# Kernel optimization log

Hardware: AMD Instinct MI355X
Metric: run time of the kernel (lower is better)

The kernel has to match this reference:

```python
import jax, jax.numpy as jnp
import numpy as np

DN = ('NCHW', 'OIHW', 'NCHW')

def conv2d(x, w, b):
    y = jax.lax.conv_general_dilated(x, w, window_strides=(1, 1), padding='SAME', dimension_numbers=DN)
    return y + b[None, :, None, None]

def setup_inputs() -> dict:
    key = jax.random.key(0)
    ks = jax.random.split(key, 8)
    C = 256
    Cq = C // 8
    B, H, W = 8, 56, 56
    fan_out_qk = Cq * 9
    fan_out_v = C * 9
    std_qk = np.sqrt(2.0 / fan_out_qk)  # kaiming_normal fan_out, relu
    std_v = np.sqrt(2.0 / fan_out_v)
    return {
        'x': jax.random.normal(ks[0], (B, C, H, W), dtype=jnp.float32),
        'wq': jax.random.normal(ks[1], (Cq, C, 3, 3), dtype=jnp.float32) * std_qk,
        'bq': jnp.zeros((Cq,), dtype=jnp.float32),
        'wk': jax.random.normal(ks[2], (Cq, C, 3, 3), dtype=jnp.float32) * std_qk,
        'bk': jnp.zeros((Cq,), dtype=jnp.float32),
        'wv': jax.random.normal(ks[3], (C, C, 3, 3), dtype=jnp.float32) * std_v,
        'bv': jnp.zeros((C,), dtype=jnp.float32),
        'gamma': jax.random.uniform(ks[4], (1,), dtype=jnp.float32) * 0.1,
    }

def reference(x, wq, bq, wk, bk, wv, bv, gamma):
    B, C, H, W = x.shape
    N = H * W
    q = conv2d(x, wq, bq).reshape(B, -1, N)   # [B, C/8, N]
    k = conv2d(x, wk, bk).reshape(B, -1, N)   # [B, C/8, N]
    v = conv2d(x, wv, bv).reshape(B, C, N)    # [B, C, N]
    # energy[b,i,j] = sum_d q[b,d,i] * k[b,d,j]  (unscaled)
    energy = jnp.einsum('bdi,bdj->bij', q, k)
    attention = jax.nn.softmax(energy, axis=-1)  # [B, N, N]
    # out[b,c,i] = sum_j v[b,c,j] * attention[b,i,j]
    out = jnp.einsum('bcj,bij->bci', v, attention).reshape(B, C, H, W)
    return gamma[0] * out + x
```

## Files before the change

### kernel.cpp

```cpp
#include <hip/hip_runtime.h>
#include <math.h>

#define B_ 8
#define C_ 256
#define H_ 56
#define W_ 56
#define N_ 3136
#define BN_ (B_*N_)
#define LOG2E 1.44269504088896340736f

typedef __attribute__((ext_vector_type(8))) short short8;
typedef __attribute__((ext_vector_type(4))) float f32x4;
typedef __attribute__((ext_vector_type(16))) float f32x16;
typedef __attribute__((ext_vector_type(4))) unsigned short u16x4;
#define MFMA16(A, Bf, Cf) __builtin_amdgcn_mfma_f32_16x16x32_bf16((A), (Bf), (Cf), 0, 0, 0)
#define MFMA32(A, Bf, Cf) __builtin_amdgcn_mfma_f32_32x32x16_bf16((A), (Bf), (Cf), 0, 0, 0)

#define XT_ELEMS (B_*58*64*256)
#define A_ELEMS  (320*2304)
#define AHI_OFF  (2*XT_ELEMS)
#define ALO_OFF  (AHI_OFF + A_ELEMS)
#define QKT_HI_OFF (ALO_OFF + A_ELEMS)
#define QKT_ELEMS  (B_*N_*64)
#define QKT_LO_OFF (QKT_HI_OFF + QKT_ELEMS)
#define VBF_OFF    (QKT_LO_OFF + QKT_ELEMS)
#define VBF_ELEMS  (B_*C_*N_)

#define QF_ELEMS (B_*196*64*8)


#define SX(col) ((((col) & 3)) ^ (((col) >> 2) & 3))
#define SWZ(r, col, c8) ((((r)*64 + (col))*4) + ((c8) ^ SX(col)))

#define PSTR 76
#define VSTR 58

__device__ inline unsigned short f2bf(float f) {
    unsigned u = __float_as_uint(f);
    unsigned r = (u + 0x7fffu + ((u >> 16) & 1u)) >> 16;
    return (unsigned short)r;
}
__device__ inline float bf2f(unsigned short h) {
    return __uint_as_float(((unsigned)h) << 16);
}
__device__ inline float exp2_hw(float x) {
    float r; asm("v_exp_f32 %0, %1" : "=v"(r) : "v"(x)); return r;
}
__device__ inline unsigned cvt_pk_bf16(float lo, float hi) {
    unsigned r; asm("v_cvt_pk_bf16_f32 %0, %1, %2" : "=v"(r) : "v"(lo), "v"(hi)); return r;
}
__device__ inline void gl_lds16(const unsigned short* g, uint4* l) {
    __builtin_amdgcn_global_load_lds(
        (const __attribute__((address_space(1))) unsigned int*)g,
        (__attribute__((address_space(3))) unsigned int*)l,
        16, 0, 0);
}

__global__ __launch_bounds__(256) void zero_pads(
    unsigned short* __restrict__ xhi, unsigned short* __restrict__ xlo)
{
    const int g = blockIdx.x*256 + threadIdx.x;
    const int half = 61440;
    unsigned short* base = (g < half) ? xhi : xlo;
    const int i = (g < half) ? g : g - half;
    const int b = i / 7680, rem = i - b*7680;
    const int slot = rem >> 5, c8 = rem & 31;
    int row, col;
    if (slot < 64)       { row = 0;  col = slot; }
    else if (slot < 128) { row = 57; col = slot - 64; }
    else if (slot < 184) { row = slot - 127; col = 0; }
    else                 { row = slot - 183; col = 57; }
    const size_t o = ((size_t)((b*58 + row)*64 + col))*256 + c8*8;
    *(uint4*)(base + o) = make_uint4(0, 0, 0, 0);
}

__global__ __launch_bounds__(256) void prep_x(
    const float* __restrict__ x,
    unsigned short* __restrict__ xhi, unsigned short* __restrict__ xlo)
{
    __shared__ float xs[64][57];
    const int cc = blockIdx.x, y = blockIdx.y, b = blockIdx.z;
    const int t = threadIdx.x;
    const int c0 = cc * 64;
    for (int idx = t; idx < 64 * 56; idx += 256) {
        const int ch = idx / 56, xc = idx - ch * 56;
        xs[ch][xc] = x[((size_t)(b*C_ + c0 + ch)*H_ + y)*W_ + xc];
    }
    __syncthreads();
    for (int idx = t; idx < 56 * 32; idx += 256) {
        const int xc = idx >> 5, chp = idx & 31;
        const float v0 = xs[2*chp][xc], v1 = xs[2*chp + 1][xc];
        const unsigned short h0 = f2bf(v0), h1 = f2bf(v1);
        const unsigned short l0 = f2bf(v0 - bf2f(h0));
        const unsigned short l1 = f2bf(v1 - bf2f(h1));
        const size_t o = ((size_t)(b*58 + y + 1) * 64 + (xc + 1)) * 256 + c0 + 2*chp;
        *(unsigned*)(xhi + o) = (unsigned)h0 | ((unsigned)h1 << 16);
        *(unsigned*)(xlo + o) = (unsigned)l0 | ((unsigned)l1 << 16);
    }
}

__global__ __launch_bounds__(256) void prep_w(
    const float* __restrict__ wq, const float* __restrict__ wk,
    const float* __restrict__ wv,
    unsigned short* __restrict__ Ahi, unsigned short* __restrict__ Alo)
{
    const int g = blockIdx.x * 256 + threadIdx.x;
    if (g >= 320 * 2304) return;
    const int m = g / 2304, k = g - m * 2304;
    const int s = k >> 8, c = k & 255;
    float w;
    if (m < 32)      w = wq[((size_t)m*C_ + c)*9 + s];
    else if (m < 64) w = wk[((size_t)(m-32)*C_ + c)*9 + s];
    else             w = wv[((size_t)(m-64)*C_ + c)*9 + s];
    const unsigned short h = f2bf(w);
    const int cc = (k >> 5) & 7, quad = (k >> 3) & 3, e = k & 7;
    const size_t o = ((((size_t)(m >> 4)*9 + s)*8 + cc)*64 + (quad*16 + (m & 15)))*8 + e;
    Ahi[o] = h;
    Alo[o] = f2bf(w - bf2f(h));
}

__global__ __launch_bounds__(256, 3) void conv_fused(
    const unsigned short* __restrict__ xhi, const unsigned short* __restrict__ xlo,
    const unsigned short* __restrict__ Ahi, const unsigned short* __restrict__ Alo,
    const float* __restrict__ bq, const float* __restrict__ bk,
    const float* __restrict__ bv,
    unsigned short* __restrict__ qkt_hi, unsigned short* __restrict__ qkt_lo,
    unsigned short* __restrict__ vbf)
{
    __shared__ uint4 SMEM[3080];
    const int b = blockIdx.x, y = blockIdx.y, z = blockIdx.z;
    const int t = threadIdx.x;
    const int w = t >> 6, L = t & 63;
    const int ln = L & 15, quad = L >> 4;

    size_t gofs[3];
#pragma unroll
    for (int i = 0; i < 3; i++) {
        const int ci = w*192 + i*64 + L;
        const int r = ci >> 8, col = (ci >> 2) & 63;
        const int c8 = (ci & 3) ^ SX(col);
        gofs[i] = ((size_t)((b*58 + y + r)*64 + col))*256 + c8*8;
    }

    if (z == 0) {
        const int wrg = w >> 1, wnt = w & 1;
        f32x4 acc[2][2];
#pragma unroll
        for (int i = 0; i < 2; i++) { acc[i][0] = (f32x4)0.0f; acc[i][1] = (f32x4)0.0f; }

#pragma unroll
        for (int i = 0; i < 3; i++) {
            gl_lds16(xhi + gofs[i], SMEM + w*192 + i*64);
            gl_lds16(xlo + gofs[i], SMEM + 768 + w*192 + i*64);
        }
        __syncthreads();

        for (int cc = 0; cc < 8; cc++) {
            const int buf = cc & 1;
            const uint4* sH = SMEM + buf*1536;
            const uint4* sL = sH + 768;
            if (cc < 7) {
                uint4* nB = SMEM + (buf^1)*1536;
#pragma unroll
                for (int i = 0; i < 3; i++) {
                    gl_lds16(xhi + gofs[i] + (cc+1)*32, nB + w*192 + i*64);
                    gl_lds16(xlo + gofs[i] + (cc+1)*32, nB + 768 + w*192 + i*64);
                }
            }
#pragma unroll
            for (int s = 0; s < 9; s++) {
                const int dx = s % 3 - 1;
                const int r = s / 3;
                short8 ah[2], al[2];
#pragma unroll
                for (int rgi = 0; rgi < 2; rgi++) {
                    const int rg = wrg*2 + rgi;
                    const size_t aoff = (((size_t)(rg*9 + s)*8 + cc)*64 + L)*8;
                    ah[rgi] = *(const short8*)(Ahi + aoff);
                    al[rgi] = *(const short8*)(Alo + aoff);
                }
#pragma unroll
                for (int nti = 0; nti < 2; nti++) {
                    const int col = (wnt*2 + nti)*16 + ln + dx + 1;
                    const int i4 = SWZ(r, col, quad);
                    const short8 bh = *(const short8*)&sH[i4];
                    const short8 bl = *(const short8*)&sL[i4];
#pragma unroll
                    for (int rgi = 0; rgi < 2; rgi++) {
                        acc[rgi][nti] = MFMA16(ah[rgi], bh, acc[rgi][nti]);
                        acc[rgi][nti] = MFMA16(ah[rgi], bl, acc[rgi][nti]);
                        acc[rgi][nti] = MFMA16(al[rgi], bh, acc[rgi][nti]);
                    }
                }
            }
            if (cc < 7) __syncthreads();
        }

#pragma unroll
        for (int rgi = 0; rgi < 2; rgi++) {
            const int rg = wrg*2 + rgi;
            const int m0 = rg*16 + quad*4;
#pragma unroll
            for (int nti = 0; nti < 2; nti++) {
                const int px = (wnt*2 + nti)*16 + ln;
                if (px >= 56) continue;
                const int pix = y*56 + px;
                u16x4 hi4, lo4;
#pragma unroll
                for (int r = 0; r < 4; r++) {
                    const int m = m0 + r;
                    const float bias = (m < 32) ? bq[m] : bk[m - 32];
                    float val = acc[rgi][nti][r] + bias;
                    if (rg < 2) val *= LOG2E;
                    const unsigned short h = f2bf(val);
                    hi4[r] = h;
                    lo4[r] = f2bf(val - bf2f(h));
                }
                size_t o;
                if (rg < 2) {
                    o = ((size_t)(b*196 + (pix >> 4))*64 + (m0 >> 3)*16 + (pix & 15))*8 + (m0 & 7);
                } else {
                    const int mk0 = m0 - 32;
                    o = (size_t)QF_ELEMS +
                        (((size_t)(b*49 + (pix >> 6))*4 + ((pix >> 4) & 3))*64
                         + (mk0 >> 3)*16 + (pix & 15))*8 + (mk0 & 7);
                }
                *(u16x4*)(qkt_hi + o) = hi4;
                *(u16x4*)(qkt_lo + o) = lo4;
            }
        }
    } else {
        f32x4 acc[4][4];
#pragma unroll
        for (int rg = 0; rg < 4; rg++)
#pragma unroll
            for (int nt = 0; nt < 4; nt++) acc[rg][nt] = (f32x4)0.0f;

#pragma unroll
        for (int i = 0; i < 3; i++)
            gl_lds16(xhi + gofs[i], SMEM + w*192 + i*64);
        __syncthreads();

        for (int cc = 0; cc < 8; cc++) {
            const int buf = cc & 1;
            const uint4* sH = SMEM + buf*768;
            if (cc < 7) {
                uint4* nB = SMEM + (buf^1)*768;
#pragma unroll
                for (int i = 0; i < 3; i++)
                    gl_lds16(xhi + gofs[i] + (cc+1)*32, nB + w*192 + i*64);
            }
#pragma unroll
            for (int s = 0; s < 9; s++) {
                const int dx = s % 3 - 1;
                const int r = s / 3;
                short8 a[4];
#pragma unroll
                for (int rg = 0; rg < 4; rg++) {
                    const size_t aoff = (((size_t)((4 + w*4 + rg)*9 + s)*8 + cc)*64 + L)*8;
                    a[rg] = *(const short8*)(Ahi + aoff);
                }
#pragma unroll
                for (int nt = 0; nt < 4; nt++) {
                    const int col = nt*16 + ln + dx + 1;
                    const short8 bf = *(const short8*)&sH[SWZ(r, col, quad)];
#pragma unroll
                    for (int rg = 0; rg < 4; rg++)
                        acc[rg][nt] = MFMA16(a[rg], bf, acc[rg][nt]);
                }
            }
            __syncthreads();
        }

        unsigned short* Vs = (unsigned short*)SMEM;
#pragma unroll
        for (int rg = 0; rg < 4; rg++)
#pragma unroll
            for (int nt = 0; nt < 4; nt++) {
                const int px = nt*16 + ln;
                if (px >= 56) continue;
#pragma unroll
                for (int r = 0; r < 4; r++) {
                    const int cl = (w*4 + rg)*16 + quad*4 + r;
                    Vs[cl*VSTR + px] = f2bf(acc[rg][nt][r] + bv[cl]);
                }
            }
        __syncthreads();
        const int p0 = y*56;
        const int hh = L >> 5, c31 = L & 31;
        const int gend = (p0 + 55) >> 4;
        for (int gi = p0 >> 4; gi <= gend; gi++) {
            const int pxl0 = gi*16 + hh*8 - p0;
            if (pxl0 >= 0 && pxl0 + 8 <= 56) {
#pragma unroll
                for (int cgk = 0; cgk < 2; cgk++) {
                    const int cg = w*2 + cgk;
                    const short8 vv = *(const short8*)&Vs[(cg*32 + c31)*VSTR + pxl0];
                    const size_t o = ((((size_t)(b*8 + cg)*49 + (gi >> 2))*4 + (gi & 3))*64 + L)*8;
                    *(short8*)(vbf + o) = vv;
                }
            }
        }
    }
}

__global__ __launch_bounds__(128, 4) void attn_flash2w(
    const unsigned short* __restrict__ qkt_hi, const unsigned short* __restrict__ qkt_lo,
    const unsigned short* __restrict__ vbf,
    const float* __restrict__ x, const float* __restrict__ gptr,
    float* __restrict__ out)
{
    __shared__ unsigned short P[2][32*PSTR];
    __shared__ float alphaL[2][32];
    __shared__ float lL[32];

    const int bx = blockIdx.x;
    const int b = bx & 7, it = bx >> 3;
    const int chalf = blockIdx.y;
    const int i_base = it * 32;
    const int t = threadIdx.x;
    const int w = t >> 6, L = t & 63;
    const int ln = L & 15, quad = L >> 4;
    const int l32 = L & 31, h32 = L >> 5;

    const unsigned short* Kf_hi = qkt_hi + QF_ELEMS;
    const unsigned short* Kf_lo = qkt_lo + QF_ELEMS;

    const size_t qoff = ((size_t)(b*196 + it*2 + w)*64 + L)*8;
    const short8 qh = *(const short8*)(qkt_hi + qoff);
    const short8 ql = *(const short8*)(qkt_lo + qoff);

    float m_run = -INFINITY, l_run = 0.0f;
    f32x16 O0 = (f32x16)0.0f, O1 = (f32x16)0.0f;
    const int cg0 = chalf*4 + w*2;
    const unsigned short* vt0 = vbf + ((size_t)(b*8 + cg0)*49)*2048 + (size_t)L*8;
    const unsigned short* vt1 = vt0 + (size_t)49*2048;
    const unsigned short* kbh = Kf_hi + (size_t)b*49*2048 + (size_t)L*8;
    const unsigned short* kbl = Kf_lo + (size_t)b*49*2048 + (size_t)L*8;

    for (int jt = 0; jt < 49; jt++) {
        const int buf = jt & 1;

        short8 Va[4], Vb[4];
#pragma unroll
        for (int s = 0; s < 4; s++) {
            Va[s] = *(const short8*)(vt0 + jt*2048 + s*512);
            Vb[s] = *(const short8*)(vt1 + jt*2048 + s*512);
        }

        f32x4 sacc[4];
#pragma unroll
        for (int tj = 0; tj < 4; tj++) {
            const short8 kh = *(const short8*)(kbh + jt*2048 + tj*512);
            const short8 kl = *(const short8*)(kbl + jt*2048 + tj*512);
            f32x4 a = (f32x4)0.0f;
            a = MFMA16(kh, qh, a);
            a = MFMA16(kh, ql, a);
            a = MFMA16(kl, qh, a);
            sacc[tj] = a;
        }
        float mt0 = fmaxf(fmaxf(sacc[0][0], sacc[0][1]), fmaxf(sacc[0][2], sacc[0][3]));
        float mt1 = fmaxf(fmaxf(sacc[1][0], sacc[1][1]), fmaxf(sacc[1][2], sacc[1][3]));
        float mt2 = fmaxf(fmaxf(sacc[2][0], sacc[2][1]), fmaxf(sacc[2][2], sacc[2][3]));
        float mt3 = fmaxf(fmaxf(sacc[3][0], sacc[3][1]), fmaxf(sacc[3][2], sacc[3][3]));
        float mx = fmaxf(fmaxf(mt0, mt1), fmaxf(mt2, mt3));
        mx = fmaxf(mx, __shfl_xor(mx, 16));
        mx = fmaxf(mx, __shfl_xor(mx, 32));

        float alpha = 1.0f;
        if (__any(mx > m_run + 8.0f)) {
            const float m_new = fmaxf(m_run, mx);
            alpha = exp2_hw(m_run - m_new);
            m_run = m_new;
        }

#pragma unroll
        for (int tj = 0; tj < 4; tj++)
#pragma unroll
            for (int r = 0; r < 4; r++)
                sacc[tj][r] = exp2_hw(sacc[tj][r] - m_run);
        float s0 = (sacc[0][0] + sacc[0][1]) + (sacc[0][2] + sacc[0][3]);
        float s1 = (sacc[1][0] + sacc[1][1]) + (sacc[1][2] + sacc[1][3]);
        float s2 = (sacc[2][0] + sacc[2][1]) + (sacc[2][2] + sacc[2][3]);
        float s3 = (sacc[3][0] + sacc[3][1]) + (sacc[3][2] + sacc[3][3]);
        float ps = (s0 + s1) + (s2 + s3);
        ps += __shfl_xor(ps, 16);
        ps += __shfl_xor(ps, 32);
        l_run = l_run * alpha + ps;

        {
            unsigned short* prow = &P[buf][(w*16 + ln)*PSTR];
#pragma unroll
            for (int tj = 0; tj < 4; tj++) {
                uint2 pp;
                pp.x = cvt_pk_bf16(sacc[tj][0], sacc[tj][1]);
                pp.y = cvt_pk_bf16(sacc[tj][2], sacc[tj][3]);
                *(uint2*)(prow + tj*16 + quad*4) = pp;
            }
        }
        if (quad == 0) alphaL[buf][w*16 + ln] = alpha;

        __syncthreads();

        const float a = alphaL[buf][l32];
        if (__any(a != 1.0f)) {
#pragma unroll
            for (int rg = 0; rg < 16; rg++) { O0[rg] *= a; O1[rg] *= a; }
        }
        short8 Bp[4];
#pragma unroll
        for (int s = 0; s < 4; s++) {
            Bp[s] = *(const short8*)&P[buf][l32*PSTR + s*16 + h32*8];
            O0 = MFMA32(Va[s], Bp[s], O0);
        }
#pragma unroll
        for (int s = 0; s < 4; s++)
            O1 = MFMA32(Vb[s], Bp[s], O1);
    }

    __syncthreads();
    if (quad == 0) lL[w*16 + ln] = l_run;
    __syncthreads();
    const float inv = gptr[0] / lL[l32];

    const int pix = i_base + l32;
#pragma unroll
    for (int g = 0; g < 2; g++) {
        const f32x16 Ot = g ? O1 : O0;
        const int cg = chalf*128 + w*64 + g*32;
#pragma unroll
        for (int reg = 0; reg < 16; reg++) {
            const int c = cg + (reg & 3) + 8*(reg >> 2) + 4*h32;
            const size_t idx = (size_t)(b*C_ + c)*N_ + pix;
            out[idx] = x[idx] + inv * Ot[reg];
        }
    }
}

extern "C" void kernel_launch(void* const* d_in, const int* in_sizes, int n_in,
                              void* d_out, int out_size, void* d_ws, size_t ws_size,
                              hipStream_t stream)
{
    (void)in_sizes; (void)n_in; (void)out_size; (void)ws_size;
    const float* x  = (const float*)d_in[0];
    const float* wq = (const float*)d_in[1];
    const float* bq = (const float*)d_in[2];
    const float* wk = (const float*)d_in[3];
    const float* bk = (const float*)d_in[4];
    const float* wv = (const float*)d_in[5];
    const float* bv = (const float*)d_in[6];
    const float* gm = (const float*)d_in[7];
    float* out = (float*)d_out;

    unsigned short* u = (unsigned short*)d_ws;
    unsigned short* xhi = u;
    unsigned short* xlo = u + XT_ELEMS;
    unsigned short* Ahi = u + AHI_OFF;
    unsigned short* Alo = u + ALO_OFF;
    unsigned short* qkt_hi = u + QKT_HI_OFF;
    unsigned short* qkt_lo = u + QKT_LO_OFF;
    unsigned short* vbf = u + VBF_OFF;

    hipLaunchKernelGGL(zero_pads, dim3(480), dim3(256), 0, stream, xhi, xlo);
    hipLaunchKernelGGL(prep_x, dim3(4, 56, 8), dim3(256), 0, stream, x, xhi, xlo);
    hipLaunchKernelGGL(prep_w, dim3(2880), dim3(256), 0, stream, wq, wk, wv, Ahi, Alo);
    hipLaunchKernelGGL(conv_fused, dim3(8, 56, 2), dim3(256), 0, stream,
                       xhi, xlo, Ahi, Alo, bq, bk, bv, qkt_hi, qkt_lo, vbf);
    hipLaunchKernelGGL(attn_flash2w, dim3(98*8, 2), dim3(128), 0, stream,
                       qkt_hi, qkt_lo, vbf, x, gm, out);
}
```

Baseline: 295.5 us.

## Restructure flash attention to single-wave blocks with 16x16 MFMA for PV

Each attention block now holds one 64-lane wave covering 16 query pixels and 128 channels, instead of two waves covering 32 pixels. The PV product now uses 16x16x32 MFMAs over 8 channel tiles, and the V layout written by the conv kernel changes to match. This drops the block-wide __syncthreads and the shared alpha/l exchange per key tile. The cost is twice as many blocks, and each block rereads K and V for only 16 queries, which doubles K/V traffic from global memory or L2.

```diff
diff --git a/kernel.cpp b/kernel.cpp
--- a/kernel.cpp
+++ b/kernel.cpp
@@ -14,7 +14,6 @@
 typedef __attribute__((ext_vector_type(16))) float f32x16;
 typedef __attribute__((ext_vector_type(4))) unsigned short u16x4;
 #define MFMA16(A, Bf, Cf) __builtin_amdgcn_mfma_f32_16x16x32_bf16((A), (Bf), (Cf), 0, 0, 0)
-#define MFMA32(A, Bf, Cf) __builtin_amdgcn_mfma_f32_32x32x16_bf16((A), (Bf), (Cf), 0, 0, 0)
 
 #define XT_ELEMS (B_*58*64*256)
 #define A_ELEMS  (320*2304)
@@ -295,8 +294,13 @@
 #pragma unroll
                 for (int cgk = 0; cgk < 2; cgk++) {
                     const int cg = w*2 + cgk;
-                    const short8 vv = *(const short8*)&Vs[(cg*32 + c31)*VSTR + pxl0];
-                    const size_t o = ((((size_t)(b*8 + cg)*49 + (gi >> 2))*4 + (gi & 3))*64 + L)*8;
+                    const int ch = cg*32 + c31;
+                    const short8 vv = *(const short8*)&Vs[ch*VSTR + pxl0];
+                    const int pix0 = p0 + pxl0;
+                    const int jt = pix0 >> 6, j6 = pix0 & 63;
+                    const int kk = j6 >> 5, qd = (j6 >> 3) & 3;
+                    const size_t o = ((((size_t)(b*16 + (ch >> 4))*49 + jt)*2 + kk)*64
+                                      + qd*16 + (ch & 15))*8;
                     *(short8*)(vbf + o) = vv;
                 }
             }
@@ -304,49 +308,43 @@
     }
 }
 
-__global__ __launch_bounds__(128, 4) void attn_flash2w(
+__global__ __launch_bounds__(64, 3) void attn_flash1w(
     const unsigned short* __restrict__ qkt_hi, const unsigned short* __restrict__ qkt_lo,
     const unsigned short* __restrict__ vbf,
     const float* __restrict__ x, const float* __restrict__ gptr,
     float* __restrict__ out)
 {
-    __shared__ unsigned short P[2][32*PSTR];
-    __shared__ float alphaL[2][32];
-    __shared__ float lL[32];
+    __shared__ unsigned short P16[16*PSTR];
 
     const int bx = blockIdx.x;
     const int b = bx & 7, it = bx >> 3;
     const int chalf = blockIdx.y;
-    const int i_base = it * 32;
     const int t = threadIdx.x;
-    const int w = t >> 6, L = t & 63;
-    const int ln = L & 15, quad = L >> 4;
-    const int l32 = L & 31, h32 = L >> 5;
+    const int ln = t & 15, quad = t >> 4;
 
     const unsigned short* Kf_hi = qkt_hi + QF_ELEMS;
     const unsigned short* Kf_lo = qkt_lo + QF_ELEMS;
 
-    const size_t qoff = ((size_t)(b*196 + it*2 + w)*64 + L)*8;
+    const size_t qoff = ((size_t)(b*196 + it)*64 + t)*8;
     const short8 qh = *(const short8*)(qkt_hi + qoff);
     const short8 ql = *(const short8*)(qkt_lo + qoff);
 
     float m_run = -INFINITY, l_run = 0.0f;
-    f32x16 O0 = (f32x16)0.0f, O1 = (f32x16)0.0f;
-    const int cg0 = chalf*4 + w*2;
-    const unsigned short* vt0 = vbf + ((size_t)(b*8 + cg0)*49)*2048 + (size_t)L*8;
-    const unsigned short* vt1 = vt0 + (size_t)49*2048;
-    const unsigned short* kbh = Kf_hi + (size_t)b*49*2048 + (size_t)L*8;
-    const unsigned short* kbl = Kf_lo + (size_t)b*49*2048 + (size_t)L*8;
+    f32x4 acc[8];
+#pragma unroll
+    for (int ctl = 0; ctl < 8; ctl++) acc[ctl] = (f32x4)0.0f;
+
+    const unsigned short* vbase = vbf + ((size_t)(b*16 + chalf*8)*49)*1024 + (size_t)t*8;
+    const unsigned short* kbh = Kf_hi + (size_t)b*49*2048 + (size_t)t*8;
+    const unsigned short* kbl = Kf_lo + (size_t)b*49*2048 + (size_t)t*8;
 
     for (int jt = 0; jt < 49; jt++) {
-        const int buf = jt & 1;
-
-        short8 Va[4], Vb[4];
-#pragma unroll
-        for (int s = 0; s < 4; s++) {
-            Va[s] = *(const short8*)(vt0 + jt*2048 + s*512);
-            Vb[s] = *(const short8*)(vt1 + jt*2048 + s*512);
-        }
+        short8 Va[8][2];
+#pragma unroll
+        for (int ctl = 0; ctl < 8; ctl++)
+#pragma unroll
+            for (int kk = 0; kk < 2; kk++)
+                Va[ctl][kk] = *(const short8*)(vbase + (size_t)ctl*49*1024 + (jt*2 + kk)*512);
 
         f32x4 sacc[4];
 #pragma unroll
@@ -389,7 +387,7 @@
         l_run = l_run * alpha + ps;
 
         {
-            unsigned short* prow = &P[buf][(w*16 + ln)*PSTR];
+            unsigned short* prow = &P16[ln*PSTR];
 #pragma unroll
             for (int tj = 0; tj < 4; tj++) {
                 uint2 pp;
@@ -398,41 +396,30 @@
                 *(uint2*)(prow + tj*16 + quad*4) = pp;
             }
         }
-        if (quad == 0) alphaL[buf][w*16 + ln] = alpha;
-
-        __syncthreads();
-
-        const float a = alphaL[buf][l32];
-        if (__any(a != 1.0f)) {
-#pragma unroll
-            for (int rg = 0; rg < 16; rg++) { O0[rg] *= a; O1[rg] *= a; }
-        }
-        short8 Bp[4];
-#pragma unroll
-        for (int s = 0; s < 4; s++) {
-            Bp[s] = *(const short8*)&P[buf][l32*PSTR + s*16 + h32*8];
-            O0 = MFMA32(Va[s], Bp[s], O0);
-        }
-#pragma unroll
-        for (int s = 0; s < 4; s++)
-            O1 = MFMA32(Vb[s], Bp[s], O1);
-    }
-
-    __syncthreads();
-    if (quad == 0) lL[w*16 + ln] = l_run;
-    __syncthreads();
-    const float inv = gptr[0] / lL[l32];
-
-    const int pix = i_base + l32;
-#pragma unroll
-    for (int g = 0; g < 2; g++) {
-        const f32x16 Ot = g ? O1 : O0;
-        const int cg = chalf*128 + w*64 + g*32;
-#pragma unroll
-        for (int reg = 0; reg < 16; reg++) {
-            const int c = cg + (reg & 3) + 8*(reg >> 2) + 4*h32;
+
+        if (__any(alpha != 1.0f)) {
+#pragma unroll
+            for (int ctl = 0; ctl < 8; ctl++) acc[ctl] *= alpha;
+        }
+
+#pragma unroll
+        for (int kk = 0; kk < 2; kk++) {
+            const short8 Bp = *(const short8*)&P16[ln*PSTR + kk*32 + quad*8];
+#pragma unroll
+            for (int ctl = 0; ctl < 8; ctl++)
+                acc[ctl] = MFMA16(Va[ctl][kk], Bp, acc[ctl]);
+        }
+    }
+
+    const float inv = gptr[0] / l_run;
+    const int pix = it*16 + ln;
+#pragma unroll
+    for (int ctl = 0; ctl < 8; ctl++) {
+#pragma unroll
+        for (int r = 0; r < 4; r++) {
+            const int c = chalf*128 + ctl*16 + quad*4 + r;
             const size_t idx = (size_t)(b*C_ + c)*N_ + pix;
-            out[idx] = x[idx] + inv * Ot[reg];
+            out[idx] = x[idx] + inv * acc[ctl][r];
         }
     }
 }
@@ -466,6 +453,6 @@
     hipLaunchKernelGGL(prep_w, dim3(2880), dim3(256), 0, stream, wq, wk, wv, Ahi, Alo);
     hipLaunchKernelGGL(conv_fused, dim3(8, 56, 2), dim3(256), 0, stream,
                        xhi, xlo, Ahi, Alo, bq, bk, bv, qkt_hi, qkt_lo, vbf);
-    hipLaunchKernelGGL(attn_flash2w, dim3(98*8, 2), dim3(128), 0, stream,
+    hipLaunchKernelGGL(attn_flash1w, dim3(196*8, 2), dim3(64), 0, stream,
                        qkt_hi, qkt_lo, vbf, x, gm, out);
 }
```

Result: slower. 366.5 us (+24.0%).

## Split attention channels into quarters and merge pad-zeroing with weight prep

Applied to the files above, without the earlier changes.

The attention kernel now launches 4 channel-quarter blocks per query tile instead of 2, so each wave accumulates one 32-channel output tile rather than two. This doubles the grid and lowers register pressure, which should raise occupancy. The cost is that the QK^T logits and softmax are recomputed twice as often. The row-sum cross-lane reduction moves out of the loop to the end, and the pad-zeroing and weight-prep kernels are merged into one launch to save a kernel launch.

```diff
diff --git a/kernel.cpp b/kernel.cpp
--- a/kernel.cpp
+++ b/kernel.cpp
@@ -56,22 +56,41 @@
         16, 0, 0);
 }
 
-__global__ __launch_bounds__(256) void zero_pads(
-    unsigned short* __restrict__ xhi, unsigned short* __restrict__ xlo)
+__global__ __launch_bounds__(256) void prep_misc(
+    unsigned short* __restrict__ xhi, unsigned short* __restrict__ xlo,
+    const float* __restrict__ wq, const float* __restrict__ wk,
+    const float* __restrict__ wv,
+    unsigned short* __restrict__ Ahi, unsigned short* __restrict__ Alo)
 {
-    const int g = blockIdx.x*256 + threadIdx.x;
-    const int half = 61440;
-    unsigned short* base = (g < half) ? xhi : xlo;
-    const int i = (g < half) ? g : g - half;
-    const int b = i / 7680, rem = i - b*7680;
-    const int slot = rem >> 5, c8 = rem & 31;
-    int row, col;
-    if (slot < 64)       { row = 0;  col = slot; }
-    else if (slot < 128) { row = 57; col = slot - 64; }
-    else if (slot < 184) { row = slot - 127; col = 0; }
-    else                 { row = slot - 183; col = 57; }
-    const size_t o = ((size_t)((b*58 + row)*64 + col))*256 + c8*8;
-    *(uint4*)(base + o) = make_uint4(0, 0, 0, 0);
+    if (blockIdx.x < 480) {
+        const int g = blockIdx.x*256 + threadIdx.x;
+        const int half = 61440;
+        unsigned short* base = (g < half) ? xhi : xlo;
+        const int i = (g < half) ? g : g - half;
+        const int b = i / 7680, rem = i - b*7680;
+        const int slot = rem >> 5, c8 = rem & 31;
+        int row, col;
+        if (slot < 64)       { row = 0;  col = slot; }
+        else if (slot < 128) { row = 57; col = slot - 64; }
+        else if (slot < 184) { row = slot - 127; col = 0; }
+        else                 { row = slot - 183; col = 57; }
+        const size_t o = ((size_t)((b*58 + row)*64 + col))*256 + c8*8;
+        *(uint4*)(base + o) = make_uint4(0, 0, 0, 0);
+    } else {
+        const int g = (blockIdx.x - 480)*256 + threadIdx.x;
+        if (g >= 320 * 2304) return;
+        const int m = g / 2304, k = g - m * 2304;
+        const int s = k >> 8, c = k & 255;
+        float w;
+        if (m < 32)      w = wq[((size_t)m*C_ + c)*9 + s];
+        else if (m < 64) w = wk[((size_t)(m-32)*C_ + c)*9 + s];
+        else             w = wv[((size_t)(m-64)*C_ + c)*9 + s];
+        const unsigned short h = f2bf(w);
+        const int cc = (k >> 5) & 7, quad = (k >> 3) & 3, e = k & 7;
+        const size_t o = ((((size_t)(m >> 4)*9 + s)*8 + cc)*64 + (quad*16 + (m & 15)))*8 + e;
+        Ahi[o] = h;
+        Alo[o] = f2bf(w - bf2f(h));
+    }
 }
 
 __global__ __launch_bounds__(256) void prep_x(
@@ -97,26 +116,6 @@
         *(unsigned*)(xhi + o) = (unsigned)h0 | ((unsigned)h1 << 16);
         *(unsigned*)(xlo + o) = (unsigned)l0 | ((unsigned)l1 << 16);
     }
-}
-
-__global__ __launch_bounds__(256) void prep_w(
-    const float* __restrict__ wq, const float* __restrict__ wk,
-    const float* __restrict__ wv,
-    unsigned short* __restrict__ Ahi, unsigned short* __restrict__ Alo)
-{
-    const int g = blockIdx.x * 256 + threadIdx.x;
-    if (g >= 320 * 2304) return;
-    const int m = g / 2304, k = g - m * 2304;
-    const int s = k >> 8, c = k & 255;
-    float w;
-    if (m < 32)      w = wq[((size_t)m*C_ + c)*9 + s];
-    else if (m < 64) w = wk[((size_t)(m-32)*C_ + c)*9 + s];
-    else             w = wv[((size_t)(m-64)*C_ + c)*9 + s];
-    const unsigned short h = f2bf(w);
-    const int cc = (k >> 5) & 7, quad = (k >> 3) & 3, e = k & 7;
-    const size_t o = ((((size_t)(m >> 4)*9 + s)*8 + cc)*64 + (quad*16 + (m & 15)))*8 + e;
-    Ahi[o] = h;
-    Alo[o] = f2bf(w - bf2f(h));
 }
 
 __global__ __launch_bounds__(256, 3) void conv_fused(
@@ -316,7 +315,7 @@
 
     const int bx = blockIdx.x;
     const int b = bx & 7, it = bx >> 3;
-    const int chalf = blockIdx.y;
+    const int cq = blockIdx.y;
     const int i_base = it * 32;
     const int t = threadIdx.x;
     const int w = t >> 6, L = t & 63;
@@ -330,23 +329,19 @@
     const short8 qh = *(const short8*)(qkt_hi + qoff);
     const short8 ql = *(const short8*)(qkt_lo + qoff);
 
-    float m_run = -INFINITY, l_run = 0.0f;
-    f32x16 O0 = (f32x16)0.0f, O1 = (f32x16)0.0f;
-    const int cg0 = chalf*4 + w*2;
-    const unsigned short* vt0 = vbf + ((size_t)(b*8 + cg0)*49)*2048 + (size_t)L*8;
-    const unsigned short* vt1 = vt0 + (size_t)49*2048;
+    float m_run = -INFINITY, l_part = 0.0f;
+    f32x16 O0 = (f32x16)0.0f;
+    const unsigned short* vt0 = vbf + ((size_t)(b*8 + cq*2 + w)*49)*2048 + (size_t)L*8;
     const unsigned short* kbh = Kf_hi + (size_t)b*49*2048 + (size_t)L*8;
     const unsigned short* kbl = Kf_lo + (size_t)b*49*2048 + (size_t)L*8;
 
     for (int jt = 0; jt < 49; jt++) {
         const int buf = jt & 1;
 
-        short8 Va[4], Vb[4];
-#pragma unroll
-        for (int s = 0; s < 4; s++) {
+        short8 Va[4];
+#pragma unroll
+        for (int s = 0; s < 4; s++)
             Va[s] = *(const short8*)(vt0 + jt*2048 + s*512);
-            Vb[s] = *(const short8*)(vt1 + jt*2048 + s*512);
-        }
 
         f32x4 sacc[4];
 #pragma unroll
@@ -383,10 +378,7 @@
         float s1 = (sacc[1][0] + sacc[1][1]) + (sacc[1][2] + sacc[1][3]);
         float s2 = (sacc[2][0] + sacc[2][1]) + (sacc[2][2] + sacc[2][3]);
         float s3 = (sacc[3][0] + sacc[3][1]) + (sacc[3][2] + sacc[3][3]);
-        float ps = (s0 + s1) + (s2 + s3);
-        ps += __shfl_xor(ps, 16);
-        ps += __shfl_xor(ps, 32);
-        l_run = l_run * alpha + ps;
+        l_part = l_part * alpha + ((s0 + s1) + (s2 + s3));
 
         {
             unsigned short* prow = &P[buf][(w*16 + ln)*PSTR];
@@ -405,35 +397,30 @@
         const float a = alphaL[buf][l32];
         if (__any(a != 1.0f)) {
 #pragma unroll
-            for (int rg = 0; rg < 16; rg++) { O0[rg] *= a; O1[rg] *= a; }
-        }
-        short8 Bp[4];
+            for (int rg = 0; rg < 16; rg++) O0[rg] *= a;
+        }
 #pragma unroll
         for (int s = 0; s < 4; s++) {
-            Bp[s] = *(const short8*)&P[buf][l32*PSTR + s*16 + h32*8];
-            O0 = MFMA32(Va[s], Bp[s], O0);
-        }
-#pragma unroll
-        for (int s = 0; s < 4; s++)
-            O1 = MFMA32(Vb[s], Bp[s], O1);
-    }
-
+            const short8 Bp = *(const short8*)&P[buf][l32*PSTR + s*16 + h32*8];
+            O0 = MFMA32(Va[s], Bp, O0);
+        }
+    }
+
+    float l_row = l_part;
+    l_row += __shfl_xor(l_row, 16);
+    l_row += __shfl_xor(l_row, 32);
     __syncthreads();
-    if (quad == 0) lL[w*16 + ln] = l_run;
+    if (quad == 0) lL[w*16 + ln] = l_row;
     __syncthreads();
     const float inv = gptr[0] / lL[l32];
 
     const int pix = i_base + l32;
-#pragma unroll
-    for (int g = 0; g < 2; g++) {
-        const f32x16 Ot = g ? O1 : O0;
-        const int cg = chalf*128 + w*64 + g*32;
-#pragma unroll
-        for (int reg = 0; reg < 16; reg++) {
-            const int c = cg + (reg & 3) + 8*(reg >> 2) + 4*h32;
-            const size_t idx = (size_t)(b*C_ + c)*N_ + pix;
-            out[idx] = x[idx] + inv * Ot[reg];
-        }
+    const int cg = cq*64 + w*32;
+#pragma unroll
+    for (int reg = 0; reg < 16; reg++) {
+        const int c = cg + (reg & 3) + 8*(reg >> 2) + 4*h32;
+        const size_t idx = (size_t)(b*C_ + c)*N_ + pix;
+        out[idx] = x[idx] + inv * O0[reg];
     }
 }
 
@@ -461,11 +448,11 @@
     unsigned short* qkt_lo = u + QKT_LO_OFF;
     unsigned short* vbf = u + VBF_OFF;
 
-    hipLaunchKernelGGL(zero_pads, dim3(480), dim3(256), 0, stream, xhi, xlo);
+    hipLaunchKernelGGL(prep_misc, dim3(3360), dim3(256), 0, stream,
+                       xhi, xlo, wq, wk, wv, Ahi, Alo);
     hipLaunchKernelGGL(prep_x, dim3(4, 56, 8), dim3(256), 0, stream, x, xhi, xlo);
-    hipLaunchKernelGGL(prep_w, dim3(2880), dim3(256), 0, stream, wq, wk, wv, Ahi, Alo);
     hipLaunchKernelGGL(conv_fused, dim3(8, 56, 2), dim3(256), 0, stream,
                        xhi, xlo, Ahi, Alo, bq, bk, bv, qkt_hi, qkt_lo, vbf);
-    hipLaunchKernelGGL(attn_flash2w, dim3(98*8, 2), dim3(128), 0, stream,
+    hipLaunchKernelGGL(attn_flash2w, dim3(98*8, 4), dim3(128), 0, stream,
                        qkt_hi, qkt_lo, vbf, x, gm, out);
 }
```

Result: slower. 341.8 us (+15.7%).
